# Kernel tuning notes

Measured on AMD Instinct MI355X. Metric: run time of the kernel, lower is better.

Reference implementation:

```python
import jax, jax.numpy as jnp
import numpy as np

V, D, NL, K, B, L, FF = 32000, 512, 4, 32, 2, 1024, 2048


def _ln(x, g, b, eps=1e-5):
    m = jnp.mean(x, axis=-1, keepdims=True)
    v = jnp.mean((x - m) ** 2, axis=-1, keepdims=True)
    return (x - m) * jax.lax.rsqrt(v + eps) * g + b


def setup_inputs() -> dict:
    key = jax.random.key(0)
    ks = jax.random.split(key, 16)
    s = 0.02
    n = lambda k, shape: jax.random.normal(k, shape, jnp.float32) * s
    inp = {
        "tokens": jax.random.randint(ks[0], (B, L), 0, V),
        "embed": n(ks[1], (V, D)),
        "ln1_g": jnp.ones((NL, D)), "ln1_b": jnp.zeros((NL, D)),
        "cp_w1": n(ks[2], (NL, D, D)), "cp_b1": jnp.zeros((NL, D)),
        "cp_w2": n(ks[3], (NL, D, K)), "cp_b2": jnp.zeros((NL, K)),
        "pos_scale": 0.5 * jnp.ones((NL,)), "content_scale": 0.5 * jnp.ones((NL,)),
        "val_w": n(ks[4], (NL, D, D)), "val_b": jnp.zeros((NL, D)),
        "oln_g": jnp.ones((NL, D)), "oln_b": jnp.zeros((NL, D)),
        "out_w": n(ks[5], (NL, D, D)), "out_b": jnp.zeros((NL, D)),
        "ln2_g": jnp.ones((NL, D)), "ln2_b": jnp.zeros((NL, D)),
        "ffn_w1": n(ks[6], (NL, D, FF)), "ffn_b1": jnp.zeros((NL, FF)),
        "ffn_w2": n(ks[7], (NL, FF, D)), "ffn_b2": jnp.zeros((NL, D)),
        "no_g": jnp.ones((D,)), "no_b": jnp.zeros((D,)),
        "head_b": jnp.zeros((V,)),
    }
    return inp


def _forward(tokens, embed, ln1_g, ln1_b, cp_w1, cp_b1, cp_w2, cp_b2,
             pos_scale, content_scale, val_w, val_b, oln_g, oln_b, out_w, out_b,
             ln2_g, ln2_b, ffn_w1, ffn_b1, ffn_w2, ffn_b2, no_g, no_b, head_b):
    Bn, Ln = tokens.shape
    Kn = cp_b2.shape[1]
    # fixed positional phases (register_buffer in torch)
    freqs = 1.0 / 10000.0 ** (jnp.arange(Kn, dtype=jnp.float32) / Kn)
    pos_phase = jnp.arange(Ln, dtype=jnp.float32)[:, None] * freqs[None, :]  # [L,K]
    inv_norm = 1.0 / jnp.sqrt(jnp.arange(1, Ln + 1, dtype=jnp.float32) * Kn)[None, :, None]
    h = embed[tokens]  # [B,L,D]
    for i in range(ln1_g.shape[0]):
        # --- DualAddressingPhasor on normed input ---
        x = _ln(h, ln1_g[i], ln1_b[i])
        cp = jnp.tanh(jnp.tanh(x @ cp_w1[i] + cp_b1[i]) @ cp_w2[i] + cp_b2[i]) * jnp.pi  # [B,L,K]
        tp = pos_scale[i] * pos_phase[None] + content_scale[i] * cp
        v = x @ val_w[i] + val_b[i]  # [B,L,D]
        c, s_ = jnp.cos(tp), jnp.sin(tp)  # [B,L,K]
        mem_r = jnp.cumsum(c[..., None] * v[:, :, None, :], axis=1)  # [B,L,K,D]
        mem_i = jnp.cumsum(s_[..., None] * v[:, :, None, :], axis=1)
        retrieved = (jnp.einsum('blkd,blk->bld', mem_r, c)
                     + jnp.einsum('blkd,blk->bld', mem_i, s_)) * inv_norm
        # phasor returns x + to_out(retrieved); block adds it back to h
        h = h + x + (_ln(retrieved, oln_g[i], oln_b[i]) @ out_w[i] + out_b[i])
        # --- FFN ---
        y = _ln(h, ln2_g[i], ln2_b[i])
        h = h + jax.nn.gelu(y @ ffn_w1[i] + ffn_b1[i], approximate=False) @ ffn_w2[i] + ffn_b2[i]
    # tied output head: head.weight = embed.weight
    return _ln(h, no_g, no_b) @ embed.T + head_b


def reference(tokens, embed, ln1_g, ln1_b, cp_w1, cp_b1, cp_w2, cp_b2,
              pos_scale, content_scale, val_w, val_b, oln_g, oln_b, out_w, out_b,
              ln2_g, ln2_b, ffn_w1, ffn_b1, ffn_w2, ffn_b2, no_g, no_b, head_b):
    return _forward(tokens, embed, ln1_g, ln1_b, cp_w1, cp_b1, cp_w2, cp_b2,
                    pos_scale, content_scale, val_w, val_b, oln_g, oln_b, out_w, out_b,
                    ln2_g, ln2_b, ffn_w1, ffn_b1, ffn_w2, ffn_b2, no_g, no_b, head_b)
```

## Files before the change

### kernel.cpp

```cpp
#include <hip/hip_runtime.h>
#include <hip/hip_bf16.h>
#include <math.h>

#define V_  32000
#define D_  512
#define NL_ 4
#define K_  32
#define B_  2
#define L_  1024
#define FF_ 2048
#define MR_ (B_ * L_)

typedef __bf16 bf16_t;
typedef __bf16 bf16x8 __attribute__((ext_vector_type(8)));
typedef float  f32x4  __attribute__((ext_vector_type(4)));

#define FLAG_TANH   1
#define FLAG_GELU   2
#define FLAG_INV    8
#define FLAG_CAUSAL 16
#define FLAG_TANHLO 32
#define FLAG_TRI    64

#define GLDS(gsrc, ldst) \
  __builtin_amdgcn_global_load_lds( \
      (const __attribute__((address_space(1))) unsigned int*)(const void*)(gsrc), \
      (__attribute__((address_space(3))) unsigned int*)(void*)(ldst), 16, 0, 0)

__global__ void gather_kernel(const int* __restrict__ tokens,
                              const float* __restrict__ embed,
                              float* __restrict__ h) {
    int row = blockIdx.x;
    int t = tokens[row];
    const float4* src = (const float4*)(embed + (size_t)t * D_);
    float4* dst = (float4*)(h + (size_t)row * D_);
    dst[threadIdx.x] = src[threadIdx.x];
}

__global__ __launch_bounds__(256) void cvt_kernel(const float* __restrict__ in,
                                                  bf16_t* __restrict__ out) {
    size_t i = ((size_t)blockIdx.x * 256 + threadIdx.x) * 8;
    float4 f0 = ((const float4*)(in + i))[0];
    float4 f1 = ((const float4*)(in + i))[1];
    bf16x8 ov;
    ov[0] = (bf16_t)f0.x; ov[1] = (bf16_t)f0.y;
    ov[2] = (bf16_t)f0.z; ov[3] = (bf16_t)f0.w;
    ov[4] = (bf16_t)f1.x; ov[5] = (bf16_t)f1.y;
    ov[6] = (bf16_t)f1.z; ov[7] = (bf16_t)f1.w;
    *(bf16x8*)(out + i) = ov;
}

__global__ void bconcat_kernel(const float* __restrict__ a,
                               const float* __restrict__ b,
                               float* __restrict__ o) {
    int i = blockIdx.x, t = threadIdx.x;
    o[(size_t)i * 2 * D_ + t]       = a[(size_t)i * D_ + t];
    o[(size_t)i * 2 * D_ + D_ + t]  = b[(size_t)i * D_ + t];
}

__global__ __launch_bounds__(256) void ln_kernel(const float* __restrict__ in,
                                                 const float* __restrict__ g,
                                                 const float* __restrict__ b,
                                                 float* __restrict__ outf,
                                                 bf16_t* __restrict__ outb) {
    int row = blockIdx.x, tid = threadIdx.x;
    const float* rp = in + (size_t)row * D_;
    float v0 = rp[tid], v1 = rp[tid + 256];
    float s = v0 + v1, q = v0 * v0 + v1 * v1;
#pragma unroll
    for (int o = 32; o > 0; o >>= 1) {
        s += __shfl_down(s, o, 64);
        q += __shfl_down(q, o, 64);
    }
    __shared__ float ss[4], sq[4];
    if ((tid & 63) == 0) { ss[tid >> 6] = s; sq[tid >> 6] = q; }
    __syncthreads();
    float ts = ss[0] + ss[1] + ss[2] + ss[3];
    float tq = sq[0] + sq[1] + sq[2] + sq[3];
    float mean = ts * (1.0f / D_);
    float var = tq * (1.0f / D_) - mean * mean;
    float rstd = rsqrtf(var + 1e-5f);
    float o0 = (v0 - mean) * rstd * g[tid] + b[tid];
    float o1 = (v1 - mean) * rstd * g[tid + 256] + b[tid + 256];
    if (outf) {
        outf[(size_t)row * D_ + tid]       = o0;
        outf[(size_t)row * D_ + tid + 256] = o1;
    }
    if (outb) {
        outb[(size_t)row * D_ + tid]       = (bf16_t)o0;
        outb[(size_t)row * D_ + tid + 256] = (bf16_t)o1;
    }
}

__global__ __launch_bounds__(256) void tconv_kernel(const float* __restrict__ in,
                                                    bf16_t* __restrict__ out,
                                                    int R, int C,
                                                    size_t inz, size_t outz) {
    __shared__ float t[32][33];
    const float* ip = in + (size_t)blockIdx.z * inz;
    bf16_t* op = out + (size_t)blockIdx.z * outz;
    int r0 = blockIdx.y * 32, c0 = blockIdx.x * 32;
    int tx = threadIdx.x & 31, ty = threadIdx.x >> 5;
#pragma unroll
    for (int rr = 0; rr < 4; ++rr)
        t[ty + rr * 8][tx] = ip[(size_t)(r0 + ty + rr * 8) * C + c0 + tx];
    __syncthreads();
#pragma unroll
    for (int rr = 0; rr < 4; ++rr)
        op[(size_t)(c0 + ty + rr * 8) * R + r0 + tx] = (bf16_t)t[tx][ty + rr * 8];
}

template<int BM, int BN, int NBUF, bool BF32>
__global__ __launch_bounds__(256) void mgemm(
    const bf16_t* __restrict__ A, const void* __restrict__ Bp,
    const float* __restrict__ bias, const float* __restrict__ res1,
    const float* __restrict__ res2, float* __restrict__ Cf,
    bf16_t* __restrict__ Cb, int M, int N, int Kd, int flags,
    long long strA, long long strB, long long strC, int swz) {
    __shared__ bf16_t sA[NBUF][BM * 32];
    __shared__ bf16_t sB[NBUF][BN * 32];
    const int tid = threadIdx.x;
    const int wave = tid >> 6, lane = tid & 63;
    const int lrow = lane & 15, quad = lane >> 4;
    int bx = blockIdx.x, by = blockIdx.y;
    if (swz) {
        int gx = gridDim.x, gy = gridDim.y;
        int nwg = gx * gy;
        int lid = by * gx + bx;
        int q = nwg >> 3, r = nwg & 7;
        int xcd = lid & 7, slot = lid >> 3;
        int base = (xcd < r) ? xcd * (q + 1) : r * (q + 1) + (xcd - r) * q;
        int nid = base + slot;
        bx = nid / gy;
        by = nid - bx * gy;
    }
    if ((flags & FLAG_TRI) && bx > by) return;
    const int m0 = by * BM, n0 = bx * BN;
    const int z = blockIdx.z;
    A += (size_t)z * strA;
    const bf16_t* Bb = (const bf16_t*)Bp + (BF32 ? 0 : (size_t)z * strB);
    const float*  Bf = (const float*)Bp  + (BF32 ? (size_t)z * strB : 0);
    constexpr int TM = BM / 32, TN = BN / 32;
    const int wm = (wave >> 1) * (BM / 2), wn = (wave & 1) * (BN / 2);
    f32x4 acc[TM][TN] = {};

    if constexpr (BF32) {
        for (int k0 = 0; k0 < Kd; k0 += 32) {
#pragma unroll
            for (int rb = 0; rb < BM / 64; ++rb) {
                int rowblk = wave * (BM / 64) + rb;
                int ml = rowblk * 16 + (lane >> 2);
                int qs = (lane & 3) ^ ((ml >> 1) & 3);
                GLDS(A + (size_t)(m0 + ml) * Kd + k0 + qs * 8, &sA[0][rowblk * 512]);
            }
#pragma unroll
            for (int rb = 0; rb < (BN * 4) / 256; ++rb) {
                int s = rb * 256 + tid;
                int nl = s >> 2, ql = s & 3;
                int qs = ql ^ ((nl >> 1) & 3);
                const float* src = Bf + (size_t)(n0 + nl) * Kd + k0 + qs * 8;
                float4 f0 = ((const float4*)src)[0];
                float4 f1 = ((const float4*)src)[1];
                bf16x8 ov;
                ov[0] = (bf16_t)f0.x; ov[1] = (bf16_t)f0.y;
                ov[2] = (bf16_t)f0.z; ov[3] = (bf16_t)f0.w;
                ov[4] = (bf16_t)f1.x; ov[5] = (bf16_t)f1.y;
                ov[6] = (bf16_t)f1.z; ov[7] = (bf16_t)f1.w;
                *(bf16x8*)(&sB[0][s * 8]) = ov;
            }
            __syncthreads();
            bf16x8 af[TM], bv[TN];
#pragma unroll
            for (int i = 0; i < TM; ++i) {
                int row = wm + i * 16 + lrow;
                af[i] = *(const bf16x8*)(&sA[0][(row * 4 + (quad ^ ((row >> 1) & 3))) * 8]);
            }
#pragma unroll
            for (int j = 0; j < TN; ++j) {
                int rown = wn + j * 16 + lrow;
                bv[j] = *(const bf16x8*)(&sB[0][(rown * 4 + (quad ^ ((rown >> 1) & 3))) * 8]);
            }
#pragma unroll
            for (int i = 0; i < TM; ++i)
#pragma unroll
                for (int j = 0; j < TN; ++j)
                    acc[i][j] = __builtin_amdgcn_mfma_f32_16x16x32_bf16(af[i], bv[j], acc[i][j], 0, 0, 0);
            __syncthreads();
        }
    } else {
        int kend = Kd;
        if (flags & FLAG_CAUSAL) { int ke = m0 + BM; kend = ke < Kd ? ke : Kd; }
        const int nk = kend >> 5;
        constexpr int NLD = BM / 64 + BN / 64;
        auto stage = [&](int t, int buf) {
            const int k0 = t << 5;
#pragma unroll
            for (int rb = 0; rb < BM / 64; ++rb) {
                int rowblk = wave * (BM / 64) + rb;
                int ml = rowblk * 16 + (lane >> 2);
                int qs = (lane & 3) ^ ((ml >> 1) & 3);
                GLDS(A + (size_t)(m0 + ml) * Kd + k0 + qs * 8, &sA[buf][rowblk * 512]);
            }
#pragma unroll
            for (int rb = 0; rb < BN / 64; ++rb) {
                int rowblk = wave * (BN / 64) + rb;
                int nl = rowblk * 16 + (lane >> 2);
                int qs = (lane & 3) ^ ((nl >> 1) & 3);
                GLDS(Bb + (size_t)(n0 + nl) * Kd + k0 + qs * 8, &sB[buf][rowblk * 512]);
            }
        };
        auto compute = [&](int buf) {
            const bf16_t* sAc = sA[buf];
            const bf16_t* sBc = sB[buf];
            bf16x8 af[TM], bv[TN];
#pragma unroll
            for (int i = 0; i < TM; ++i) {
                int row = wm + i * 16 + lrow;
                af[i] = *(const bf16x8*)(sAc + (row * 4 + (quad ^ ((row >> 1) & 3))) * 8);
            }
#pragma unroll
            for (int j = 0; j < TN; ++j) {
                int rown = wn + j * 16 + lrow;
                bv[j] = *(const bf16x8*)(sBc + (rown * 4 + (quad ^ ((rown >> 1) & 3))) * 8);
            }
#pragma unroll
            for (int i = 0; i < TM; ++i)
#pragma unroll
                for (int j = 0; j < TN; ++j)
                    acc[i][j] = __builtin_amdgcn_mfma_f32_16x16x32_bf16(af[i], bv[j], acc[i][j], 0, 0, 0);
        };
        if constexpr (NBUF == 2) {
            stage(0, 0);
            int cur = 0;
            for (int t = 0; t < nk; ++t) {
                if (t + 1 < nk) {
                    stage(t + 1, cur ^ 1);
                    asm volatile("s_waitcnt vmcnt(%0)" :: "n"(NLD) : "memory");
                } else {
                    asm volatile("s_waitcnt vmcnt(0)" ::: "memory");
                }
                __builtin_amdgcn_s_barrier();
                compute(cur);
                asm volatile("s_waitcnt lgkmcnt(0)" ::: "memory");
                __builtin_amdgcn_s_barrier();
                cur ^= 1;
            }
        } else {
            for (int t = 0; t < NBUF - 1 && t < nk; ++t) stage(t, t & (NBUF - 1));
            for (int t = 0; t < nk; ++t) {
                const int nxt = t + NBUF - 1;
                if (nxt < nk) stage(nxt, nxt & (NBUF - 1));
                const int issued_last = (nxt < nk) ? nxt : nk - 1;
                const int ahead = issued_last - t;
                switch (ahead) {
                  case 0: asm volatile("s_waitcnt vmcnt(0)" ::: "memory"); break;
                  case 1: asm volatile("s_waitcnt vmcnt(%0)" :: "n"(1 * NLD) : "memory"); break;
                  case 2: asm volatile("s_waitcnt vmcnt(%0)" :: "n"(2 * NLD) : "memory"); break;
                  default: asm volatile("s_waitcnt vmcnt(%0)" :: "n"(3 * NLD) : "memory"); break;
                }
                __builtin_amdgcn_s_barrier();
                compute(t & (NBUF - 1));
                asm volatile("s_waitcnt lgkmcnt(0)" ::: "memory");
                __builtin_amdgcn_s_barrier();
            }
        }
    }

    const size_t zo = (size_t)z * strC;
#pragma unroll
    for (int i = 0; i < TM; ++i) {
#pragma unroll
        for (int reg = 0; reg < 4; ++reg) {
            int m = m0 + wm + i * 16 + quad * 4 + reg;
            float rs = (flags & FLAG_INV) ? rsqrtf((float)(m + 1) * (float)K_) : 1.0f;
#pragma unroll
            for (int j = 0; j < TN; ++j) {
                int n = n0 + wn + j * 16 + lrow;
                float vv = acc[i][j][reg];
                if (bias) vv += bias[n];
                vv *= rs;
                if (flags & FLAG_TANH) vv = tanhf(vv);
                else if (flags & FLAG_GELU) vv = 0.5f * vv * (1.0f + erff(vv * 0.7071067811865476f));
                else if (flags & FLAG_TANHLO) { if (n < D_) vv = tanhf(vv); }
                if ((flags & FLAG_TRI) && n > m) vv = 0.f;
                size_t idx = zo + (size_t)m * N + n;
                if (res1) vv += res1[idx];
                if (res2) vv += res2[idx];
                if (Cf) Cf[idx] = vv;
                if (Cb) Cb[idx] = (bf16_t)vv;
            }
        }
    }
}

__global__ void phase_kernel(const float* __restrict__ t1,
                             const float* __restrict__ w2,
                             const float* __restrict__ b2,
                             const float* __restrict__ ps,
                             const float* __restrict__ cs,
                             int layer,
                             bf16_t* __restrict__ csb) {
    int row = blockIdx.x;
    int l = row & (L_ - 1);
    int tid = threadIdx.x;
    int k = tid & 31, hh = tid >> 5;
    const float* tr = t1 + (size_t)row * (2 * D_);
    float acc = 0.f;
    for (int d = hh * 256; d < hh * 256 + 256; ++d)
        acc = fmaf(tr[d], w2[d * K_ + k], acc);
    __shared__ float red[64];
    red[tid] = acc;
    __syncthreads();
    if (hh == 0) {
        float zz = red[k] + red[k + 32] + b2[k];
        float cp = tanhf(zz) * 3.14159265358979323846f;
        float freq = expf(-(float)k * (9.210340371976184f / (float)K_));
        float tp = ps[layer] * (float)l * freq + cs[layer] * cp;
        csb[(size_t)row * 64 + k]      = (bf16_t)cosf(tp);
        csb[(size_t)row * 64 + 32 + k] = (bf16_t)sinf(tp);
    }
}

extern "C" void kernel_launch(void* const* d_in, const int* in_sizes, int n_in,
                              void* d_out, int out_size, void* d_ws, size_t ws_size,
                              hipStream_t stream) {
    const int*   tokens        = (const int*)d_in[0];
    const float* embed         = (const float*)d_in[1];
    const float* ln1_g         = (const float*)d_in[2];
    const float* ln1_b         = (const float*)d_in[3];
    const float* cp_w1         = (const float*)d_in[4];
    const float* cp_b1         = (const float*)d_in[5];
    const float* cp_w2         = (const float*)d_in[6];
    const float* cp_b2         = (const float*)d_in[7];
    const float* pos_scale     = (const float*)d_in[8];
    const float* content_scale = (const float*)d_in[9];
    const float* val_w         = (const float*)d_in[10];
    const float* val_b         = (const float*)d_in[11];
    const float* oln_g         = (const float*)d_in[12];
    const float* oln_b         = (const float*)d_in[13];
    const float* out_w         = (const float*)d_in[14];
    const float* out_b         = (const float*)d_in[15];
    const float* ln2_g         = (const float*)d_in[16];
    const float* ln2_b         = (const float*)d_in[17];
    const float* ffn_w1        = (const float*)d_in[18];
    const float* ffn_b1        = (const float*)d_in[19];
    const float* ffn_w2        = (const float*)d_in[20];
    const float* ffn_b2        = (const float*)d_in[21];
    const float* no_g          = (const float*)d_in[22];
    const float* no_b          = (const float*)d_in[23];
    const float* head_b        = (const float*)d_in[24];
    float* out = (float*)d_out;

    float* h   = out;
    float* x   = h  + (size_t)MR_ * D_;
    float* t1v = x  + (size_t)MR_ * D_;
    float* r   = t1v + (size_t)MR_ * 2 * D_;
    bf16_t* x_bf  = (bf16_t*)(r + (size_t)MR_ * D_);
    bf16_t* r_bf  = x_bf  + (size_t)MR_ * D_;
    bf16_t* y_bf  = r_bf  + (size_t)MR_ * D_;
    bf16_t* ff_bf = y_bf  + (size_t)MR_ * D_;
    bf16_t* sc_bf = ff_bf + (size_t)MR_ * FF_;
    bf16_t* vT_bf = sc_bf + (size_t)B_ * L_ * L_;
    bf16_t* csb   = vT_bf + (size_t)B_ * D_ * L_;
    bf16_t* wvT   = csb   + (size_t)MR_ * 64;
    bf16_t* owT   = wvT   + (size_t)NL_ * 2 * D_ * D_;
    bf16_t* f1T   = owT   + (size_t)NL_ * D_ * D_;
    bf16_t* f2T   = f1T   + (size_t)NL_ * FF_ * D_;
    float*  b1v   = (float*)(f2T + (size_t)NL_ * D_ * FF_);
    bf16_t* hn_bf = (bf16_t*)d_ws;
    bf16_t* emb_bf = hn_bf + (size_t)MR_ * D_;
    const bool big_ws =
        ws_size >= ((size_t)MR_ * D_ + (size_t)V_ * D_) * sizeof(bf16_t);

    gather_kernel<<<MR_, 128, 0, stream>>>(tokens, embed, h);

    tconv_kernel<<<dim3(16, 16, NL_), 256, 0, stream>>>(cp_w1, wvT, D_, D_, (size_t)D_ * D_, (size_t)2 * D_ * D_);
    tconv_kernel<<<dim3(16, 16, NL_), 256, 0, stream>>>(val_w, wvT + (size_t)D_ * D_, D_, D_, (size_t)D_ * D_, (size_t)2 * D_ * D_);
    bconcat_kernel<<<NL_, 512, 0, stream>>>(cp_b1, val_b, b1v);
    tconv_kernel<<<dim3(16, 16, NL_), 256, 0, stream>>>(out_w, owT, D_, D_, (size_t)D_ * D_, (size_t)D_ * D_);
    tconv_kernel<<<dim3(64, 16, NL_), 256, 0, stream>>>(ffn_w1, f1T, D_, FF_, (size_t)D_ * FF_, (size_t)D_ * FF_);
    tconv_kernel<<<dim3(16, 64, NL_), 256, 0, stream>>>(ffn_w2, f2T, FF_, D_, (size_t)FF_ * D_, (size_t)FF_ * D_);
    if (big_ws)
        cvt_kernel<<<(V_ * D_) / 2048, 256, 0, stream>>>(embed, emb_bf);

    for (int i = 0; i < NL_; ++i) {
        ln_kernel<<<MR_, 256, 0, stream>>>(h, ln1_g + i * D_, ln1_b + i * D_, x, x_bf);
        mgemm<64, 64, 4, false><<<dim3(16, 32, 1), 256, 0, stream>>>(
            x_bf, wvT + (size_t)i * 2 * D_ * D_, b1v + (size_t)i * 2 * D_,
            nullptr, nullptr, t1v, nullptr, MR_, 2 * D_, D_, FLAG_TANHLO, 0, 0, 0, 1);
        phase_kernel<<<MR_, 64, 0, stream>>>(
            t1v, cp_w2 + (size_t)i * D_ * K_, cp_b2 + i * K_,
            pos_scale, content_scale, i, csb);
        tconv_kernel<<<dim3(16, 32, B_), 256, 0, stream>>>(
            t1v + D_, vT_bf, L_, 2 * D_, (size_t)L_ * 2 * D_, (size_t)D_ * L_);
        mgemm<64, 64, 2, false><<<dim3(L_ / 64, L_ / 64, B_), 256, 0, stream>>>(
            csb, csb, nullptr, nullptr, nullptr, nullptr, sc_bf,
            L_, L_, 64, FLAG_TRI,
            (long long)L_ * 64, (long long)L_ * 64, (long long)L_ * L_, 0);
        mgemm<64, 64, 4, false><<<dim3(8, 16, B_), 256, 0, stream>>>(
            sc_bf, vT_bf, nullptr, nullptr, nullptr, r, nullptr,
            L_, D_, L_, FLAG_INV | FLAG_CAUSAL,
            (long long)L_ * L_, (long long)D_ * L_, (long long)L_ * D_, 1);
        ln_kernel<<<MR_, 256, 0, stream>>>(r, oln_g + i * D_, oln_b + i * D_, nullptr, r_bf);
        mgemm<64, 64, 4, false><<<dim3(8, 32, 1), 256, 0, stream>>>(
            r_bf, owT + (size_t)i * D_ * D_, out_b + i * D_,
            h, x, h, nullptr, MR_, D_, D_, 0, 0, 0, 0, 1);
        ln_kernel<<<MR_, 256, 0, stream>>>(h, ln2_g + i * D_, ln2_b + i * D_, nullptr, y_bf);
        mgemm<128, 128, 4, false><<<dim3(16, 16, 1), 256, 0, stream>>>(
            y_bf, f1T + (size_t)i * FF_ * D_, ffn_b1 + i * FF_,
            nullptr, nullptr, nullptr, ff_bf, MR_, FF_, D_, FLAG_GELU, 0, 0, 0, 1);
        mgemm<64, 64, 4, false><<<dim3(8, 32, 1), 256, 0, stream>>>(
            ff_bf, f2T + (size_t)i * D_ * FF_, ffn_b2 + i * D_,
            h, nullptr, h, nullptr, MR_, D_, FF_, 0, 0, 0, 0, 1);
    }

    ln_kernel<<<MR_, 256, 0, stream>>>(h, no_g, no_b, nullptr, hn_bf);
    if (big_ws) {
        mgemm<128, 128, 2, false><<<dim3(V_ / 128, MR_ / 128, 1), 256, 0, stream>>>(
            hn_bf, emb_bf, head_b, nullptr, nullptr, out, nullptr,
            MR_, V_, D_, 0, 0, 0, 0, 1);
    } else {
        mgemm<128, 128, 1, true><<<dim3(V_ / 128, MR_ / 128, 1), 256, 0, stream>>>(
            hn_bf, embed, head_b, nullptr, nullptr, out, nullptr,
            MR_, V_, D_, 0, 0, 0, 0, 1);
    }
}
```

Before: 1.489 ms.

## Split-K FFN down-projection, triple-buffer head GEMM, batch phase rows per block

Splits the FFN second GEMM (K=2048) into two half-K partial GEMMs over a z-dimension, then adds the partials, bias and residual in a new sumk kernel, so that GEMM launches twice as many blocks. Adds a 3-stage buffering path to mgemm and uses it for the vocab head GEMM. Reworks phase_kernel to handle four rows per 256-thread block instead of one row per 64-thread block. The split-K path costs an extra fp32 partial buffer write and read plus one more launch, and the 3-buffer path uses more LDS.

```diff
diff --git a/kernel.cpp b/kernel.cpp
--- a/kernel.cpp
+++ b/kernel.cpp
@@ -21,6 +21,7 @@
 #define FLAG_CAUSAL 16
 #define FLAG_TANHLO 32
 #define FLAG_TRI    64
+#define FLAG_HALFK  128
 
 #define GLDS(gsrc, ldst) \
   __builtin_amdgcn_global_load_lds( \
@@ -56,6 +57,22 @@
     int i = blockIdx.x, t = threadIdx.x;
     o[(size_t)i * 2 * D_ + t]       = a[(size_t)i * D_ + t];
     o[(size_t)i * 2 * D_ + D_ + t]  = b[(size_t)i * D_ + t];
+}
+
+__global__ __launch_bounds__(128) void sumk_kernel(const float* __restrict__ p0,
+                                                   const float* __restrict__ p1,
+                                                   const float* __restrict__ bias,
+                                                   float* __restrict__ h) {
+    size_t o = (size_t)blockIdx.x * D_ + threadIdx.x * 4;
+    float4 a = *(const float4*)(p0 + o);
+    float4 c = *(const float4*)(p1 + o);
+    float4 hb = *(const float4*)(h + o);
+    float4 bb = *(const float4*)(bias + threadIdx.x * 4);
+    hb.x += a.x + c.x + bb.x;
+    hb.y += a.y + c.y + bb.y;
+    hb.z += a.z + c.z + bb.z;
+    hb.w += a.w + c.w + bb.w;
+    *(float4*)(h + o) = hb;
 }
 
 __global__ __launch_bounds__(256) void ln_kernel(const float* __restrict__ in,
@@ -190,6 +207,7 @@
     } else {
         int kend = Kd;
         if (flags & FLAG_CAUSAL) { int ke = m0 + BM; kend = ke < Kd ? ke : Kd; }
+        if (flags & FLAG_HALFK) kend = Kd >> 1;
         const int nk = kend >> 5;
         constexpr int NLD = BM / 64 + BN / 64;
         auto stage = [&](int t, int buf) {
@@ -244,6 +262,27 @@
                 asm volatile("s_waitcnt lgkmcnt(0)" ::: "memory");
                 __builtin_amdgcn_s_barrier();
                 cur ^= 1;
+            }
+        } else if constexpr (NBUF == 3) {
+            stage(0, 0);
+            if (nk > 1) stage(1, 1);
+            int b0 = 0;
+            for (int t = 0; t < nk; ++t) {
+                const int nxt = t + 2;
+                if (nxt < nk) {
+                    int bn = b0 + 2; if (bn >= 3) bn -= 3;
+                    stage(nxt, bn);
+                }
+                const int last = (nxt < nk) ? nxt : nk - 1;
+                const int ahead = last - t;
+                if (ahead >= 2)      asm volatile("s_waitcnt vmcnt(%0)" :: "n"(2 * NLD) : "memory");
+                else if (ahead == 1) asm volatile("s_waitcnt vmcnt(%0)" :: "n"(1 * NLD) : "memory");
+                else                 asm volatile("s_waitcnt vmcnt(0)" ::: "memory");
+                __builtin_amdgcn_s_barrier();
+                compute(b0);
+                asm volatile("s_waitcnt lgkmcnt(0)" ::: "memory");
+                __builtin_amdgcn_s_barrier();
+                b0 = (b0 == 2) ? 0 : b0 + 1;
             }
         } else {
             for (int t = 0; t < NBUF - 1 && t < nk; ++t) stage(t, t & (NBUF - 1));
@@ -293,26 +332,27 @@
     }
 }
 
-__global__ void phase_kernel(const float* __restrict__ t1,
+__global__ __launch_bounds__(256) void phase_kernel(const float* __restrict__ t1,
                              const float* __restrict__ w2,
                              const float* __restrict__ b2,
                              const float* __restrict__ ps,
                              const float* __restrict__ cs,
                              int layer,
                              bf16_t* __restrict__ csb) {
-    int row = blockIdx.x;
+    int tid = threadIdx.x;
+    int rl = tid >> 6;
+    int k = tid & 31, hh = (tid >> 5) & 1;
+    int row = blockIdx.x * 4 + rl;
     int l = row & (L_ - 1);
-    int tid = threadIdx.x;
-    int k = tid & 31, hh = tid >> 5;
     const float* tr = t1 + (size_t)row * (2 * D_);
     float acc = 0.f;
     for (int d = hh * 256; d < hh * 256 + 256; ++d)
         acc = fmaf(tr[d], w2[d * K_ + k], acc);
-    __shared__ float red[64];
+    __shared__ float red[256];
     red[tid] = acc;
     __syncthreads();
     if (hh == 0) {
-        float zz = red[k] + red[k + 32] + b2[k];
+        float zz = red[rl * 64 + k] + red[rl * 64 + 32 + k] + b2[k];
         float cp = tanhf(zz) * 3.14159265358979323846f;
         float freq = expf(-(float)k * (9.210340371976184f / (float)K_));
         float tp = ps[layer] * (float)l * freq + cs[layer] * cp;
@@ -367,6 +407,7 @@
     bf16_t* f1T   = owT   + (size_t)NL_ * D_ * D_;
     bf16_t* f2T   = f1T   + (size_t)NL_ * FF_ * D_;
     float*  b1v   = (float*)(f2T + (size_t)NL_ * D_ * FF_);
+    float*  pK    = b1v + (size_t)NL_ * 2 * D_;
     bf16_t* hn_bf = (bf16_t*)d_ws;
     bf16_t* emb_bf = hn_bf + (size_t)MR_ * D_;
     const bool big_ws =
@@ -388,7 +429,7 @@
         mgemm<64, 64, 4, false><<<dim3(16, 32, 1), 256, 0, stream>>>(
             x_bf, wvT + (size_t)i * 2 * D_ * D_, b1v + (size_t)i * 2 * D_,
             nullptr, nullptr, t1v, nullptr, MR_, 2 * D_, D_, FLAG_TANHLO, 0, 0, 0, 1);
-        phase_kernel<<<MR_, 64, 0, stream>>>(
+        phase_kernel<<<MR_ / 4, 256, 0, stream>>>(
             t1v, cp_w2 + (size_t)i * D_ * K_, cp_b2 + i * K_,
             pos_scale, content_scale, i, csb);
         tconv_kernel<<<dim3(16, 32, B_), 256, 0, stream>>>(
@@ -409,14 +450,17 @@
         mgemm<128, 128, 4, false><<<dim3(16, 16, 1), 256, 0, stream>>>(
             y_bf, f1T + (size_t)i * FF_ * D_, ffn_b1 + i * FF_,
             nullptr, nullptr, nullptr, ff_bf, MR_, FF_, D_, FLAG_GELU, 0, 0, 0, 1);
-        mgemm<64, 64, 4, false><<<dim3(8, 32, 1), 256, 0, stream>>>(
-            ff_bf, f2T + (size_t)i * D_ * FF_, ffn_b2 + i * D_,
-            h, nullptr, h, nullptr, MR_, D_, FF_, 0, 0, 0, 0, 1);
+        mgemm<64, 64, 4, false><<<dim3(8, 32, 2), 256, 0, stream>>>(
+            ff_bf, f2T + (size_t)i * D_ * FF_, nullptr,
+            nullptr, nullptr, pK, nullptr, MR_, D_, FF_, FLAG_HALFK,
+            (long long)(FF_ / 2), (long long)(FF_ / 2), (long long)MR_ * D_, 1);
+        sumk_kernel<<<MR_, 128, 0, stream>>>(
+            pK, pK + (size_t)MR_ * D_, ffn_b2 + i * D_, h);
     }
 
     ln_kernel<<<MR_, 256, 0, stream>>>(h, no_g, no_b, nullptr, hn_bf);
     if (big_ws) {
-        mgemm<128, 128, 2, false><<<dim3(V_ / 128, MR_ / 128, 1), 256, 0, stream>>>(
+        mgemm<128, 128, 3, false><<<dim3(V_ / 128, MR_ / 128, 1), 256, 0, stream>>>(
             hn_bf, emb_bf, head_b, nullptr, nullptr, out, nullptr,
             MR_, V_, D_, 0, 0, 0, 0, 1);
     } else {
```

New measurement: 1.426 ms. 1.04x faster.
